# Kernel tuning notes

Hardware: AMD Instinct MI355X
Metric: run time of the kernel (lower is better)

The kernel has to match this reference:

```python
import jax, jax.numpy as jnp
import numpy as np
from jax import lax

LEAK = 0.2
EPS = 1e-5
T = 20  # sequence_length


def _lrelu(x):
    return jnp.where(x >= 0, x, LEAK * x)


def _deconv(x, w, stride=2, k=4, p=1):
    # PyTorch ConvTranspose2d(weight [in,out,kH,kW], stride=2, pad=1) equivalent:
    # flip kernel spatially, swap in/out channels, use lhs_dilation.
    wt = jnp.flip(w, (2, 3)).transpose(1, 0, 2, 3)  # OIHW
    pad = k - 1 - p
    return lax.conv_general_dilated(
        x, wt, window_strides=(1, 1), padding=[(pad, pad), (pad, pad)],
        lhs_dilation=(stride, stride),
        dimension_numbers=('NCHW', 'OIHW', 'NCHW'))


def _bn(x, g, b):
    # BatchNorm2d, training mode (batch statistics, biased variance)
    m = x.mean((0, 2, 3), keepdims=True)
    v = x.var((0, 2, 3), keepdims=True)
    return (x - m) * lax.rsqrt(v + EPS) * g[None, :, None, None] + b[None, :, None, None]


def setup_inputs() -> dict:
    B, CD, MD, H, FF = 64, 128, 128, 256, 512
    ks = jax.random.split(jax.random.key(0), 32)
    rn = lambda k, sh, s=0.02: (s * jax.random.normal(k, sh)).astype(jnp.float32)
    return {
        'z_content': jax.random.normal(ks[0], (B, CD), jnp.float32),
        'z_motion': jax.random.normal(ks[1], (B, MD), jnp.float32),
        'W_h': rn(ks[2], (H, CD + MD)), 'b_h': jnp.zeros((H,), jnp.float32),
        'W_c': rn(ks[3], (H, CD + MD)), 'b_c': jnp.zeros((H,), jnp.float32),
        'W_ih': rn(ks[4], (4 * H, H)), 'W_hh': rn(ks[5], (4 * H, H)),
        'b_ih': jnp.zeros((4 * H,), jnp.float32), 'b_hh': jnp.zeros((4 * H,), jnp.float32),
        'W_f': rn(ks[6], (FF, H)), 'b_f': jnp.zeros((FF,), jnp.float32),
        'init_in': rn(ks[7], (1, H), 0.1),
        'fc_W': rn(ks[8], (256 * 4 * 4, FF + CD)), 'fc_b': jnp.zeros((256 * 16,), jnp.float32),
        'w0': rn(ks[9], (256, 128, 4, 4)), 'g0': jnp.ones((128,), jnp.float32), 'be0': jnp.zeros((128,), jnp.float32),
        'w1': rn(ks[10], (128, 64, 4, 4)), 'g1': jnp.ones((64,), jnp.float32), 'be1': jnp.zeros((64,), jnp.float32),
        'w2': rn(ks[11], (64, 32, 4, 4)), 'g2': jnp.ones((32,), jnp.float32), 'be2': jnp.zeros((32,), jnp.float32),
        'wf': rn(ks[12], (32, 1, 4, 4)), 'bf': jnp.zeros((1,), jnp.float32),
    }


def reference(z_content, z_motion, W_h, b_h, W_c, b_c, W_ih, W_hh, b_ih, b_hh,
              W_f, b_f, init_in, fc_W, fc_b, w0, g0, be0, w1, g1, be1,
              w2, g2, be2, wf, bf):
    B = z_content.shape[0]
    z = jnp.concatenate([z_content, z_motion], axis=-1)
    h0 = z @ W_h.T + b_h  # [B,H]
    c0 = z @ W_c.T + b_c
    x0 = jnp.broadcast_to(init_in, (B, init_in.shape[1]))
    bias = b_ih + b_hh

    def step(carry, _):
        x, h, c = carry
        gates = x @ W_ih.T + h @ W_hh.T + bias  # [B,4H], torch gate order i,f,g,o
        i, f, g, o = jnp.split(gates, 4, axis=-1)
        c_new = jax.nn.sigmoid(f) * c + jax.nn.sigmoid(i) * jnp.tanh(g)
        h_new = jax.nn.sigmoid(o) * jnp.tanh(c_new)
        return (h_new, h_new, c_new), h_new

    _, outs = lax.scan(step, (x0, h0, c0), None, length=T)  # [T,B,H]
    outs = outs.transpose(1, 0, 2)  # [B,T,H]

    ff = _lrelu(outs @ W_f.T + b_f)  # [B,T,FF]
    zc = jnp.broadcast_to(z_content[:, None, :], (B, T, z_content.shape[1]))
    feat = jnp.concatenate([ff, zc], axis=-1).reshape(B * T, -1)  # [B*T, FF+CD]

    h = _lrelu(feat @ fc_W.T + fc_b).reshape(B * T, 256, 4, 4)
    h = _lrelu(_bn(_deconv(h, w0), g0, be0))   # [B*T,128,8,8]
    h = _lrelu(_bn(_deconv(h, w1), g1, be1))   # [B*T,64,16,16]
    h = _lrelu(_bn(_deconv(h, w2), g2, be2))   # [B*T,32,32,32]
    out = jax.nn.sigmoid(_deconv(h, wf) + bf[None, :, None, None])  # [B*T,1,64,64]
    return out.reshape(B, T, *out.shape[1:])
```

## Files before the change

### kernel.cpp

```cpp
#include <hip/hip_runtime.h>
#include <hip/hip_bf16.h>
#include <math.h>

typedef __hip_bfloat16 bf16;
typedef __attribute__((ext_vector_type(8))) short bf16x8;
typedef __attribute__((ext_vector_type(4))) float f32x4;
typedef __attribute__((ext_vector_type(2))) float f32x2;

#define LRELU(v) ((v) > 0.f ? (v) : 0.2f*(v))

__device__ __forceinline__ float sig_f(float x){ return 1.f/(1.f + __expf(-x)); }
__device__ __forceinline__ float tanh_f(float x){
  float ax = fabsf(x);
  float e = __expf(-2.f*ax);
  float t = (1.f - e)/(1.f + e);
  return x >= 0.f ? t : -t;
}
__device__ __forceinline__ ushort bfbits(float v){
  bf16 b = __float2bfloat16(v);
  return *(ushort*)&b;
}
__device__ __forceinline__ uint bfpack(float a, float b){
  return (uint)bfbits(a) | ((uint)bfbits(b) << 16);
}
__device__ __forceinline__ float bflo(uint u){ return __uint_as_float(u << 16); }
__device__ __forceinline__ float bfhi(uint u){ return __uint_as_float(u & 0xffff0000u); }

template<int CI, int CO>
__device__ __forceinline__ void wprep_body(const float* __restrict__ w,
                                           ushort* __restrict__ wpn, int e){
  constexpr int K = 4*CI, KF = K/32, MMW2 = CO/16;
  if (e >= 16*CI*CO) return;
  int j  = e & 7;
  int lk = (e >> 3) & 3;
  int lm = (e >> 5) & 15;
  int r3 = e >> 9;
  int kf = r3 % KF; int r4 = r3 / KF;
  int m  = r4 % MMW2; int p = r4 / MMW2;
  int k  = kf*32 + lk*8 + j;
  int t  = k / CI, ci = k % CI;
  int co = m*16 + lm;
  int py = p >> 1, px = p & 1, dy = t >> 1, dx = t & 1;
  int ky = (py ? 0 : 1) + 2*dy;
  int kx = (px ? 0 : 1) + 2*dx;
  wpn[e] = bfbits(w[((ci*CO + co)*4 + ky)*4 + kx]);
}

__global__ __launch_bounds__(256) void k_prep(
    const float* __restrict__ W_h, const float* __restrict__ W_c,
    float* __restrict__ WhT, float* __restrict__ WcT,
    const float* __restrict__ fc_W, ushort* __restrict__ wpfc,
    const float* __restrict__ W_f, ushort* __restrict__ wpff,
    const float* __restrict__ Wih, const float* __restrict__ Whh,
    uint4* __restrict__ Whq8, uint4* __restrict__ Wsq8, float* __restrict__ stats,
    const float* __restrict__ b_ih, const float* __restrict__ b_hh,
    const float* __restrict__ init_in,
    float4* __restrict__ xg4, float4* __restrict__ bias4,
    const float* __restrict__ w0, ushort* __restrict__ wp0,
    const float* __restrict__ w1, ushort* __restrict__ wp1,
    const float* __restrict__ w2, ushort* __restrict__ wp2,
    const float* __restrict__ wf, ushort* __restrict__ wfb)
{
  __shared__ float t[32][33];
  __shared__ float4 red[4];
  const int b = blockIdx.x, tid = threadIdx.x;

  if (b < 128) {
    const float* src = (b < 64) ? W_h : W_c;
    float* dst = (b < 64) ? WhT : WcT;
    int bb = b & 63;
    int c0 = (bb & 7)*32, r0 = (bb >> 3)*32;
    int tx = tid & 31, ty = tid >> 5;
    #pragma unroll
    for (int i = 0; i < 4; ++i)
      t[ty+8*i][tx] = src[(size_t)(r0+ty+8*i)*256 + c0+tx];
    __syncthreads();
    #pragma unroll
    for (int i = 0; i < 4; ++i)
      dst[(size_t)(c0+ty+8*i)*256 + r0+tx] = t[tx][ty+8*i];
    return;
  }
  if (b < 10368) {
    int i = (b - 128)*256 + tid;
    if (i < 2621440) wpfc[i] = bfbits(fc_W[i]);
    return;
  }
  if (b < 10880) {
    int i = (b - 10368)*256 + tid;
    if (i < 131072) wpff[i] = bfbits(W_f[i]);
    return;
  }
  if (b < 10944) {
    int k4 = b - 10880, j = tid;
    if (k4 < 2) { int i = k4*256 + j; if (i < 448) stats[i] = 0.f; }
    uint h4[4], s4[4];
    #pragma unroll
    for (int d = 0; d < 4; ++d) {
      int k = 4*k4 + d;
      float hi = Whh[j*256+k],       hf = Whh[(256+j)*256+k];
      float hg = Whh[(512+j)*256+k], ho = Whh[(768+j)*256+k];
      float ii = Wih[j*256+k],       iff = Wih[(256+j)*256+k];
      float ig = Wih[(512+j)*256+k], io = Wih[(768+j)*256+k];
      int lo = __builtin_amdgcn_cvt_pk_fp8_f32(hi, hf, 0, false);
      h4[d] = (uint)__builtin_amdgcn_cvt_pk_fp8_f32(hg, ho, lo, true);
      lo = __builtin_amdgcn_cvt_pk_fp8_f32(hi+ii, hf+iff, 0, false);
      s4[d] = (uint)__builtin_amdgcn_cvt_pk_fp8_f32(hg+ig, ho+io, lo, true);
    }
    Whq8[k4*256+j] = make_uint4(h4[0], h4[1], h4[2], h4[3]);
    Wsq8[k4*256+j] = make_uint4(s4[0], s4[1], s4[2], s4[3]);
    return;
  }
  if (b < 11200) {
    int bb = b - 10944, tt = tid;
    float v = init_in[tt];
    float p0 = v * Wih[bb*256 + tt];
    float p1 = v * Wih[(256+bb)*256 + tt];
    float p2 = v * Wih[(512+bb)*256 + tt];
    float p3 = v * Wih[(768+bb)*256 + tt];
    #pragma unroll
    for (int o = 32; o; o >>= 1) {
      p0 += __shfl_xor(p0, o); p1 += __shfl_xor(p1, o);
      p2 += __shfl_xor(p2, o); p3 += __shfl_xor(p3, o);
    }
    int lane = tt & 63, wid = tt >> 6;
    if (lane == 0) red[wid] = make_float4(p0,p1,p2,p3);
    __syncthreads();
    if (tt == 0) {
      float4 bi = make_float4(b_ih[bb]+b_hh[bb], b_ih[256+bb]+b_hh[256+bb],
                              b_ih[512+bb]+b_hh[512+bb], b_ih[768+bb]+b_hh[768+bb]);
      bias4[bb] = bi;
      float4 a = bi;
      #pragma unroll
      for (int w = 0; w < 4; ++w) { a.x += red[w].x; a.y += red[w].y; a.z += red[w].z; a.w += red[w].w; }
      xg4[bb] = a;
    }
    return;
  }
  if (b < 13248) { wprep_body<256,128>(w0, wp0, (b - 11200)*256 + tid); return; }
  if (b < 13760) { wprep_body<128,64>(w1, wp1, (b - 13248)*256 + tid); return; }
  if (b < 13888) { wprep_body<64,32>(w2, wp2, (b - 13760)*256 + tid); return; }
  {
    int e = (b - 13888)*256 + tid;
    if (e < 512) {
      int tt = e >> 5, ci = e & 31;
      wfb[tt*32 + ci] = bfbits(wf[ci*16 + tt]);
    }
  }
}

__global__ __launch_bounds__(256) void k_h0c0(const float* __restrict__ zc, const float* __restrict__ zm,
                      const float* __restrict__ WhT, const float* __restrict__ WcT,
                      const float* __restrict__ b_h, const float* __restrict__ b_c,
                      float* __restrict__ h, float* __restrict__ c){
  __shared__ float zs[256];
  int b = blockIdx.x, j = threadIdx.x;
  zs[j] = (j < 128) ? zc[b*128 + j] : zm[b*128 + (j-128)];
  __syncthreads();
  float ah = b_h[j], ac = b_c[j];
  #pragma unroll 4
  for (int k = 0; k < 256; ++k) {
    float zv = zs[k];
    ah = fmaf(zv, WhT[k*256 + j], ah);
    ac = fmaf(zv, WcT[k*256 + j], ac);
  }
  h[b*256+j] = ah; c[b*256+j] = ac;
}

__global__ __launch_bounds__(1024) void k_lstm_all(
    const uint4* __restrict__ Whq8, const uint4* __restrict__ Wsq8,
    const float4* __restrict__ xg4, const float4* __restrict__ bias4,
    const float* __restrict__ h0, const float* __restrict__ c0,
    ushort* __restrict__ outsb){
  __shared__ float hs[256];
  __shared__ float4 part[3][256];
  const int b = blockIdx.x, tid = threadIdx.x;
  const int j = tid & 255, kq = tid >> 8;
  float cj = 0.f;
  if (kq == 0) { hs[j] = h0[b*256 + j]; cj = c0[b*256 + j]; }
  __syncthreads();
  for (int t = 0; t < 20; ++t) {
    const uint4* __restrict__ Wp = ((t == 0) ? Whq8 : Wsq8) + (size_t)(kq*16)*256 + j;
    float4 a = make_float4(0.f, 0.f, 0.f, 0.f);
    #pragma unroll 8
    for (int kk = 0; kk < 16; ++kk) {
      uint4 wv = Wp[(size_t)kk*256];
      const float* __restrict__ hb = &hs[kq*64 + 4*kk];
      {
        f32x2 pif = __builtin_amdgcn_cvt_pk_f32_fp8((int)wv.x, false);
        f32x2 pgo = __builtin_amdgcn_cvt_pk_f32_fp8((int)wv.x, true);
        float hv = hb[0];
        a.x = fmaf(hv, pif[0], a.x); a.y = fmaf(hv, pif[1], a.y);
        a.z = fmaf(hv, pgo[0], a.z); a.w = fmaf(hv, pgo[1], a.w);
      }
      {
        f32x2 pif = __builtin_amdgcn_cvt_pk_f32_fp8((int)wv.y, false);
        f32x2 pgo = __builtin_amdgcn_cvt_pk_f32_fp8((int)wv.y, true);
        float hv = hb[1];
        a.x = fmaf(hv, pif[0], a.x); a.y = fmaf(hv, pif[1], a.y);
        a.z = fmaf(hv, pgo[0], a.z); a.w = fmaf(hv, pgo[1], a.w);
      }
      {
        f32x2 pif = __builtin_amdgcn_cvt_pk_f32_fp8((int)wv.z, false);
        f32x2 pgo = __builtin_amdgcn_cvt_pk_f32_fp8((int)wv.z, true);
        float hv = hb[2];
        a.x = fmaf(hv, pif[0], a.x); a.y = fmaf(hv, pif[1], a.y);
        a.z = fmaf(hv, pgo[0], a.z); a.w = fmaf(hv, pgo[1], a.w);
      }
      {
        f32x2 pif = __builtin_amdgcn_cvt_pk_f32_fp8((int)wv.w, false);
        f32x2 pgo = __builtin_amdgcn_cvt_pk_f32_fp8((int)wv.w, true);
        float hv = hb[3];
        a.x = fmaf(hv, pif[0], a.x); a.y = fmaf(hv, pif[1], a.y);
        a.z = fmaf(hv, pgo[0], a.z); a.w = fmaf(hv, pgo[1], a.w);
      }
    }
    if (kq) part[kq-1][j] = a;
    __syncthreads();
    if (kq == 0) {
      float4 p1 = part[0][j], p2 = part[1][j], p3 = part[2][j];
      float4 bb = (t == 0) ? xg4[j] : bias4[j];
      a.x += p1.x + p2.x + p3.x + bb.x;
      a.y += p1.y + p2.y + p3.y + bb.y;
      a.z += p1.z + p2.z + p3.z + bb.z;
      a.w += p1.w + p2.w + p3.w + bb.w;
      float ig = sig_f(a.x), fg = sig_f(a.y), gg = tanh_f(a.z), og = sig_f(a.w);
      cj = fmaf(fg, cj, ig*gg);
      float hj = og * tanh_f(cj);
      outsb[(b*20 + t)*256 + j] = bfbits(hj);
      hs[j] = hj;
    }
    __syncthreads();
  }
}

__global__ __launch_bounds__(256) void k_ff_m(
    const ushort* __restrict__ A, const ushort* __restrict__ W,
    const float* __restrict__ bias, const float* __restrict__ zc,
    ushort* __restrict__ C)
{
  constexpr int K = 256, BK = 64, NK = K/BK, BM = 128, BN = 64;
  constexpr int RS = 72;
  constexpr int NCF = BN/16;
  constexpr int AC = 4, WC = 2;

  __shared__ __align__(16) ushort Al[2][BM*RS];
  __shared__ __align__(16) ushort Wl[2][BN*RS];

  const int tid = threadIdx.x;
  const int col0 = blockIdx.x * BN, row0 = blockIdx.y * BM;
  const int w = tid >> 6, l = tid & 63, lm = l & 15, lk = l >> 4;

  f32x4 acc[NCF][2];
  #pragma unroll
  for (int m = 0; m < NCF; ++m)
    #pragma unroll
    for (int s = 0; s < 2; ++s)
      acc[m][s] = (f32x4){0.f,0.f,0.f,0.f};

  uint4 ar[AC], wr[WC];

  #define LOADG(kt) { \
    _Pragma("unroll") \
    for (int i = 0; i < AC; ++i) { \
      int chunk = tid + i*256; \
      int rl = chunk >> 3, kc = chunk & 7; \
      ar[i] = *(const uint4*)&A[(size_t)(row0+rl)*K + (kt)*BK + kc*8]; \
    } \
    _Pragma("unroll") \
    for (int i = 0; i < WC; ++i) { \
      int chunk = tid + i*256; \
      int co = chunk >> 3, kc = chunk & 7; \
      wr[i] = *(const uint4*)&W[(size_t)(col0+co)*K + (kt)*BK + kc*8]; \
    } }

  #define STOREL(buf) { \
    _Pragma("unroll") \
    for (int i = 0; i < AC; ++i) { \
      int chunk = tid + i*256; \
      int rl = chunk >> 3, kc = chunk & 7; \
      *(uint4*)&Al[buf][rl*RS + kc*8] = ar[i]; \
    } \
    _Pragma("unroll") \
    for (int i = 0; i < WC; ++i) { \
      int chunk = tid + i*256; \
      int co = chunk >> 3, kc = chunk & 7; \
      *(uint4*)&Wl[buf][co*RS + kc*8] = wr[i]; \
    } }

  LOADG(0);
  STOREL(0);
  int cur = 0;
  for (int kt = 0; kt < NK; ++kt) {
    if (kt + 1 < NK) LOADG(kt + 1);
    __syncthreads();
    #pragma unroll
    for (int kf = 0; kf < 2; ++kf) {
      bf16x8 bfr[2];
      #pragma unroll
      for (int s = 0; s < 2; ++s)
        bfr[s] = *(bf16x8*)&Al[cur][(w*32 + s*16 + lm)*RS + kf*32 + lk*8];
      #pragma unroll
      for (int m = 0; m < NCF; ++m) {
        bf16x8 afr = *(bf16x8*)&Wl[cur][(m*16 + lm)*RS + kf*32 + lk*8];
        acc[m][0] = __builtin_amdgcn_mfma_f32_16x16x32_bf16(afr, bfr[0], acc[m][0], 0, 0, 0);
        acc[m][1] = __builtin_amdgcn_mfma_f32_16x16x32_bf16(afr, bfr[1], acc[m][1], 0, 0, 0);
      }
    }
    if (kt + 1 < NK) STOREL(cur ^ 1);
    cur ^= 1;
  }

  #pragma unroll
  for (int m = 0; m < NCF; ++m) {
    #pragma unroll
    for (int s = 0; s < 2; ++s) {
      int row = row0 + w*32 + s*16 + lm;
      f32x4 v = acc[m][s];
      int u0 = col0 + m*16 + lk*4;
      union { ushort u[4]; uint2 q; } pk;
      #pragma unroll
      for (int j = 0; j < 4; ++j)
        pk.u[j] = bfbits(LRELU(v[j] + bias[u0+j]));
      *(uint2*)&C[(size_t)row*640 + u0] = pk.q;
    }
  }
  {
    int base = ((int)blockIdx.y*8 + (int)blockIdx.x)*2048 + tid;
    #pragma unroll
    for (int i = 0; i < 8; ++i) {
      int e = base + i*256;
      int r = e >> 7, c2 = e & 127;
      C[r*640 + 512 + c2] = bfbits(zc[(r/20)*128 + c2]);
    }
  }
  #undef LOADG
  #undef STOREL
}

__global__ __launch_bounds__(256) void k_gemm_fc_m(
    const ushort* __restrict__ A, const ushort* __restrict__ W,
    const float* __restrict__ bias, ushort* __restrict__ C)
{
  constexpr int K = 640, BK = 64, NK = K/BK, BM = 128, BN = 64;
  constexpr int RS = 72;
  constexpr int NCF = BN/16;
  constexpr int AC = 4, WC = 2;

  __shared__ __align__(16) ushort Al[2][BM*RS];
  __shared__ __align__(16) ushort Wl[2][BN*RS];

  const int tid = threadIdx.x;
  const int col0 = blockIdx.x * BN, row0 = blockIdx.y * BM;
  const int w = tid >> 6, l = tid & 63, lm = l & 15, lk = l >> 4;

  f32x4 acc[NCF][2];
  #pragma unroll
  for (int m = 0; m < NCF; ++m)
    #pragma unroll
    for (int s = 0; s < 2; ++s)
      acc[m][s] = (f32x4){0.f,0.f,0.f,0.f};

  uint4 ar[AC], wr[WC];

  #define LOADG(kt) { \
    _Pragma("unroll") \
    for (int i = 0; i < AC; ++i) { \
      int chunk = tid + i*256; \
      int rl = chunk >> 3, kc = chunk & 7; \
      ar[i] = *(const uint4*)&A[(size_t)(row0+rl)*K + (kt)*BK + kc*8]; \
    } \
    _Pragma("unroll") \
    for (int i = 0; i < WC; ++i) { \
      int chunk = tid + i*256; \
      int co = chunk >> 3, kc = chunk & 7; \
      wr[i] = *(const uint4*)&W[(size_t)(col0+co)*K + (kt)*BK + kc*8]; \
    } }

  #define STOREL(buf) { \
    _Pragma("unroll") \
    for (int i = 0; i < AC; ++i) { \
      int chunk = tid + i*256; \
      int rl = chunk >> 3, kc = chunk & 7; \
      *(uint4*)&Al[buf][rl*RS + kc*8] = ar[i]; \
    } \
    _Pragma("unroll") \
    for (int i = 0; i < WC; ++i) { \
      int chunk = tid + i*256; \
      int co = chunk >> 3, kc = chunk & 7; \
      *(uint4*)&Wl[buf][co*RS + kc*8] = wr[i]; \
    } }

  LOADG(0);
  STOREL(0);
  int cur = 0;
  for (int kt = 0; kt < NK; ++kt) {
    if (kt + 1 < NK) LOADG(kt + 1);
    __syncthreads();
    #pragma unroll
    for (int kf = 0; kf < 2; ++kf) {
      bf16x8 bfr[2];
      #pragma unroll
      for (int s = 0; s < 2; ++s)
        bfr[s] = *(bf16x8*)&Al[cur][(w*32 + s*16 + lm)*RS + kf*32 + lk*8];
      #pragma unroll
      for (int m = 0; m < NCF; ++m) {
        bf16x8 afr = *(bf16x8*)&Wl[cur][(m*16 + lm)*RS + kf*32 + lk*8];
        acc[m][0] = __builtin_amdgcn_mfma_f32_16x16x32_bf16(afr, bfr[0], acc[m][0], 0, 0, 0);
        acc[m][1] = __builtin_amdgcn_mfma_f32_16x16x32_bf16(afr, bfr[1], acc[m][1], 0, 0, 0);
      }
    }
    if (kt + 1 < NK) STOREL(cur ^ 1);
    cur ^= 1;
  }

  #pragma unroll
  for (int m = 0; m < NCF; ++m) {
    #pragma unroll
    for (int s = 0; s < 2; ++s) {
      int row = row0 + w*32 + s*16 + lm;
      f32x4 v = acc[m][s];
      #pragma unroll
      for (int j = 0; j < 4; ++j) {
        int u = col0 + m*16 + lk*4 + j;
        float val = LRELU(v[j] + bias[u]);
        C[((size_t)row << 12) + ((size_t)(u & 15) << 8) + (u >> 4)] = bfbits(val);
      }
    }
  }
  #undef LOADG
  #undef STOREL
}

template<int CI, int CO, int HI>
__global__ __attribute__((amdgpu_flat_work_group_size(256, 256), amdgpu_waves_per_eu(2, 4)))
void k_dcv(
    const ushort* __restrict__ in, const ushort* __restrict__ wp,
    ushort* __restrict__ out, float* __restrict__ gsum, float* __restrict__ gsq)
{
  constexpr int WI = HI, HO = 2*HI, WO = 2*WI;
  constexpr int K = 4*CI, BK = 64, NK = K/BK, KFT = K/32;
  constexpr int BSP = 128;
  constexpr int RS = 72;
  constexpr int NCF = CO/32;
  constexpr int COH = CO/2;
  constexpr int AC = BSP/32;

  __shared__ __align__(16) ushort Al[2][BSP*RS];
  __shared__ float s_sum[COH], s_sq[COH];

  const int tid = threadIdx.x;
  const int sp0 = blockIdx.x * BSP;
  const int p  = blockIdx.y;
  const int coz = blockIdx.z;
  const int py = p >> 1, px = p & 1;
  const int w  = tid >> 6, l = tid & 63;
  const int lm = l & 15, lk = l >> 4;

  if (tid < COH) { s_sum[tid] = 0.f; s_sq[tid] = 0.f; }

  f32x4 acc[NCF][2];
  #pragma unroll
  for (int m = 0; m < NCF; ++m)
    #pragma unroll
    for (int s = 0; s < 2; ++s)
      acc[m][s] = (f32x4){0.f,0.f,0.f,0.f};

  uint4 ar[AC];
  const ushort* wpb = wp + (size_t)(p*(CO/16) + coz*NCF)*KFT*512;

  #define LOADT(kt) { \
    int t = ((kt)*BK)/CI, ci0 = ((kt)*BK)%CI; \
    int dy = t >> 1, dx = t & 1; \
    _Pragma("unroll") \
    for (int i = 0; i < AC; ++i) { \
      int chunk = tid + i*256; \
      int rl = chunk >> 3, kc = chunk & 7; \
      int r = sp0 + rl; \
      int n = r / (HI*WI), rem = r % (HI*WI); \
      int oy = rem / WI, ox = rem % WI; \
      int iy = oy + py - dy, ix = ox + px - dx; \
      if ((unsigned)iy < (unsigned)HI && (unsigned)ix < (unsigned)WI) \
        ar[i] = *(const uint4*)&in[((((size_t)n*HI + iy)*WI + ix)*CI) + ci0 + kc*8]; \
      else ar[i] = make_uint4(0,0,0,0); \
    } }

  #define STORET(buf) { \
    _Pragma("unroll") \
    for (int i = 0; i < AC; ++i) { \
      int chunk = tid + i*256; \
      int rl = chunk >> 3, kc = chunk & 7; \
      *(uint4*)&Al[buf][rl*RS + kc*8] = ar[i]; \
    } }

  LOADT(0);
  STORET(0);
  bf16x8 afrN[NCF];
  #pragma unroll
  for (int m = 0; m < NCF; ++m)
    afrN[m] = *(const bf16x8*)&wpb[((size_t)m*KFT)*512 + lm*32 + lk*8];
  int cur = 0;
  for (int kt = 0; kt < NK; ++kt) {
    if (kt + 1 < NK) LOADT(kt + 1);
    __syncthreads();
    #pragma unroll
    for (int kf = 0; kf < 2; ++kf) {
      const int ktg = kt*2 + kf;
      bf16x8 afr[NCF];
      #pragma unroll
      for (int m = 0; m < NCF; ++m) afr[m] = afrN[m];
      if (ktg + 1 < KFT) {
        #pragma unroll
        for (int m = 0; m < NCF; ++m)
          afrN[m] = *(const bf16x8*)&wpb[((size_t)m*KFT + ktg + 1)*512 + lm*32 + lk*8];
      }
      bf16x8 bfr[2];
      #pragma unroll
      for (int s = 0; s < 2; ++s)
        bfr[s] = *(bf16x8*)&Al[cur][(w*32 + s*16 + lm)*RS + kf*32 + lk*8];
      #pragma unroll
      for (int m = 0; m < NCF; ++m) {
        acc[m][0] = __builtin_amdgcn_mfma_f32_16x16x32_bf16(afr[m], bfr[0], acc[m][0], 0, 0, 0);
        acc[m][1] = __builtin_amdgcn_mfma_f32_16x16x32_bf16(afr[m], bfr[1], acc[m][1], 0, 0, 0);
      }
    }
    if (kt + 1 < NK) STORET(cur ^ 1);
    cur ^= 1;
  }

  #pragma unroll
  for (int m = 0; m < NCF; ++m) {
    float s1[4] = {0,0,0,0}, s2[4] = {0,0,0,0};
    #pragma unroll
    for (int s = 0; s < 2; ++s) {
      f32x4 v = acc[m][s];
      #pragma unroll
      for (int j = 0; j < 4; ++j) { s1[j] += v[j]; s2[j] += v[j]*v[j]; }
    }
    #pragma unroll
    for (int j = 0; j < 4; ++j) {
      float a = s1[j], b = s2[j];
      #pragma unroll
      for (int o = 1; o < 16; o <<= 1) { a += __shfl_xor(a, o); b += __shfl_xor(b, o); }
      if (lm == 0) {
        atomicAdd(&s_sum[m*16 + lk*4 + j], a);
        atomicAdd(&s_sq [m*16 + lk*4 + j], b);
      }
    }
  }
  #pragma unroll
  for (int s = 0; s < 2; ++s) {
    int sp = sp0 + w*32 + s*16 + lm;
    int n = sp / (HI*WI), rem = sp % (HI*WI);
    int y = 2*(rem / WI) + py, x = 2*(rem % WI) + px;
    size_t ob = (((size_t)n*HO + y)*WO + x)*CO + coz*COH + lk*4;
    #pragma unroll
    for (int m = 0; m < NCF; ++m) {
      f32x4 v = acc[m][s];
      union { ushort u[4]; uint2 q; } pk;
      pk.u[0] = bfbits(v[0]); pk.u[1] = bfbits(v[1]);
      pk.u[2] = bfbits(v[2]); pk.u[3] = bfbits(v[3]);
      *(uint2*)&out[ob + m*16] = pk.q;
    }
  }
  __syncthreads();
  for (int cc = tid; cc < COH; cc += 256) {
    atomicAdd(&gsum[coz*COH + cc], s_sum[cc]);
    atomicAdd(&gsq[coz*COH + cc],  s_sq[cc]);
  }
  #undef LOADT
  #undef STORET
}

template<int CI, int CO, int HI>
__global__ __attribute__((amdgpu_flat_work_group_size(512, 512), amdgpu_waves_per_eu(2, 4)))
void k_dcvim(
    const ushort* __restrict__ in, const ushort* __restrict__ wp,
    const float* __restrict__ gsumP, const float* __restrict__ gsqP,
    const float* __restrict__ gP, const float* __restrict__ beP, float invNP,
    ushort* __restrict__ out, float* __restrict__ gsum, float* __restrict__ gsq)
{
  constexpr int WI = HI, HO = 2*HI, WO = 2*WI;
  constexpr int K = 4*CI;
  constexpr int KF = K/32;
  constexpr int PAD = HI + 2;
  constexpr int CICH = CI/8;
  constexpr int MMW2 = CO/16;
  constexpr int SFTH = HI*WI/32;

  __shared__ __align__(16) ushort Ain[PAD*PAD*CI];
  __shared__ float s_sum[CO], s_sq[CO];
  __shared__ float s_scale[CI], s_shift[CI];

  const int tid = threadIdx.x;
  const int n = blockIdx.x;
  const int w = tid >> 6, l = tid & 63, lm = l & 15, lk = l >> 4;
  const int p = w >> 1, py = p >> 1, px = p & 1, ph = w & 1;

  if (tid < CO) { s_sum[tid] = 0.f; s_sq[tid] = 0.f; }
  if (tid >= 512-CI) {
    int c = tid - (512-CI);
    float m = gsumP[c]*invNP;
    float v = gsqP[c]*invNP - m*m;
    float sc = gP[c]*rsqrtf(v + 1e-5f);
    s_scale[c] = sc;
    s_shift[c] = beP[c] - m*sc;
  }
  __syncthreads();

  const ushort* inb = in + (size_t)n * HI * WI * CI;
  constexpr int NPCH = PAD*PAD*CICH;
  for (int e = tid; e < NPCH; e += 512) {
    int ci8 = e % CICH; int sp = e / CICH;
    int c = sp % PAD, r = sp / PAD;
    int chS = ci8 ^ (c & 7);
    if (r >= 1 && r <= HI && c >= 1 && c <= WI) {
      uint4 u = *(const uint4*)&inb[(((size_t)(r-1)*WI + (c-1))*CI) + ci8*8];
      int ci0 = ci8*8;
      float4 sc0 = *(const float4*)&s_scale[ci0];
      float4 sc1 = *(const float4*)&s_scale[ci0+4];
      float4 sh0 = *(const float4*)&s_shift[ci0];
      float4 sh1 = *(const float4*)&s_shift[ci0+4];
      float v0 = LRELU(fmaf(bflo(u.x), sc0.x, sh0.x));
      float v1 = LRELU(fmaf(bfhi(u.x), sc0.y, sh0.y));
      float v2 = LRELU(fmaf(bflo(u.y), sc0.z, sh0.z));
      float v3 = LRELU(fmaf(bfhi(u.y), sc0.w, sh0.w));
      float v4 = LRELU(fmaf(bflo(u.z), sc1.x, sh1.x));
      float v5 = LRELU(fmaf(bfhi(u.z), sc1.y, sh1.y));
      float v6 = LRELU(fmaf(bflo(u.w), sc1.z, sh1.z));
      float v7 = LRELU(fmaf(bfhi(u.w), sc1.w, sh1.w));
      uint4 o;
      o.x = (uint)bfpack(v0, v1);
      o.y = (uint)bfpack(v2, v3);
      o.z = (uint)bfpack(v4, v5);
      o.w = (uint)bfpack(v6, v7);
      ((uint4*)Ain)[(r*PAD + c)*CICH + chS] = o;
    } else {
      ((uint4*)Ain)[(r*PAD + c)*CICH + chS] = make_uint4(0,0,0,0);
    }
  }
  __syncthreads();

  f32x4 acc[MMW2][SFTH];
  #pragma unroll
  for (int m = 0; m < MMW2; ++m)
    #pragma unroll
    for (int sf = 0; sf < SFTH; ++sf)
      acc[m][sf] = (f32x4){0.f,0.f,0.f,0.f};

  const ushort* wpb = wp + (size_t)(p*MMW2)*KF*512;
  bf16x8 afrN[MMW2];
  #pragma unroll
  for (int m = 0; m < MMW2; ++m)
    afrN[m] = *(const bf16x8*)&wpb[((size_t)m*KF)*512 + lm*32 + lk*8];
  #pragma unroll
  for (int kf = 0; kf < KF; ++kf) {
    const int t = (kf*32)/CI, cib = (kf*32)%CI;
    const int dy = t >> 1, dx = t & 1;
    bf16x8 afr[MMW2];
    #pragma unroll
    for (int m = 0; m < MMW2; ++m) afr[m] = afrN[m];
    if (kf + 1 < KF) {
      #pragma unroll
      for (int m = 0; m < MMW2; ++m)
        afrN[m] = *(const bf16x8*)&wpb[((size_t)m*KF + (kf+1))*512 + lm*32 + lk*8];
    }
    const int ch = (cib >> 3) + lk;
    #pragma unroll
    for (int sf = 0; sf < SFTH; ++sf) {
      int s = (ph*SFTH + sf)*16 + lm;
      int y = s / WI, x = s % WI;
      int r = y + py - dy + 1, c = x + px - dx + 1;
      bf16x8 bfr = *(const bf16x8*)&Ain[((r*PAD + c)*CICH + (ch ^ (c & 7)))*8];
      #pragma unroll
      for (int m = 0; m < MMW2; ++m)
        acc[m][sf] = __builtin_amdgcn_mfma_f32_16x16x32_bf16(afr[m], bfr, acc[m][sf], 0, 0, 0);
    }
  }

  float s1[MMW2][4], s2[MMW2][4];
  #pragma unroll
  for (int m = 0; m < MMW2; ++m)
    #pragma unroll
    for (int j = 0; j < 4; ++j) { s1[m][j] = 0.f; s2[m][j] = 0.f; }

  #pragma unroll
  for (int sf = 0; sf < SFTH; ++sf) {
    int s = (ph*SFTH + sf)*16 + lm;
    int y = 2*(s / WI) + py, x = 2*(s % WI) + px;
    size_t ob = (((size_t)n*HO + y)*WO + x)*CO + lk*4;
    #pragma unroll
    for (int m = 0; m < MMW2; ++m) {
      f32x4 v = acc[m][sf];
      union { ushort u[4]; uint2 q; } pk;
      #pragma unroll
      for (int j = 0; j < 4; ++j) {
        pk.u[j] = bfbits(v[j]);
        s1[m][j] += v[j];
        s2[m][j] += v[j]*v[j];
      }
      *(uint2*)&out[ob + m*16] = pk.q;
    }
  }

  #pragma unroll
  for (int m = 0; m < MMW2; ++m) {
    #pragma unroll
    for (int j = 0; j < 4; ++j) {
      float a = s1[m][j], b = s2[m][j];
      #pragma unroll
      for (int o = 1; o < 16; o <<= 1) { a += __shfl_xor(a, o); b += __shfl_xor(b, o); }
      if (lm == 0) {
        atomicAdd(&s_sum[m*16 + lk*4 + j], a);
        atomicAdd(&s_sq [m*16 + lk*4 + j], b);
      }
    }
  }

  __syncthreads();
  for (int cc = tid; cc < CO; cc += 512) {
    atomicAdd(&gsum[cc], s_sum[cc]);
    atomicAdd(&gsq[cc],  s_sq[cc]);
  }
}

__global__ __launch_bounds__(256) void k_final(
    const ushort* __restrict__ in, const ushort* __restrict__ wfb,
    const float* __restrict__ gsumP, const float* __restrict__ gsqP,
    const float* __restrict__ gP, const float* __restrict__ beP, float invNP,
    const float* __restrict__ bfb, float* __restrict__ outp)
{
  constexpr int CI=32, HI=32, WI=32, HO=64, WO=64, SPLIT=4, HOq=HO/SPLIT;
  constexpr int RMAX = 10;
  constexpr int DP = 20;
  __shared__ float Dl[RMAX*32*DP];
  __shared__ float s_scale[CI], s_shift[CI];

  const int tid = threadIdx.x, bid = blockIdx.x;
  const int n = bid % 1280, q = bid / 1280;
  const int y0 = q * HOq;
  const int rows_lo = max(0, y0/2 - 1);
  const int rows_hi = min(HI-1, (y0 + HOq)/2);
  const int nrows = rows_hi - rows_lo + 1;

  if (tid < CI) {
    float m = gsumP[tid]*invNP;
    float v = gsqP[tid]*invNP - m*m;
    float sc = gP[tid]*rsqrtf(v + 1e-5f);
    s_scale[tid] = sc;
    s_shift[tid] = beP[tid] - m*sc;
  }
  __syncthreads();

  const int w = tid >> 6, l = tid & 63, lm = l & 15, lk = l >> 4;
  const bf16x8 afr = *(const bf16x8*)&wfb[lm*32 + lk*8];
  const float4 sc0 = *(const float4*)&s_scale[lk*8];
  const float4 sc1 = *(const float4*)&s_scale[lk*8+4];
  const float4 sh0 = *(const float4*)&s_shift[lk*8];
  const float4 sh1 = *(const float4*)&s_shift[lk*8+4];

  const ushort* inb = in + (size_t)n * HI * WI * CI;
  const int ngrp = nrows * 2;
  for (int g = w; g < ngrp; g += 4) {
    int px = g*16 + lm;
    int rl = px >> 5, ix = px & 31;
    uint4 u = *(const uint4*)&inb[(((size_t)(rows_lo+rl)*WI + ix)*CI) + lk*8];
    float v0 = LRELU(fmaf(bflo(u.x), sc0.x, sh0.x));
    float v1 = LRELU(fmaf(bfhi(u.x), sc0.y, sh0.y));
    float v2 = LRELU(fmaf(bflo(u.y), sc0.z, sh0.z));
    float v3 = LRELU(fmaf(bfhi(u.y), sc0.w, sh0.w));
    float v4 = LRELU(fmaf(bflo(u.z), sc1.x, sh1.x));
    float v5 = LRELU(fmaf(bfhi(u.z), sc1.y, sh1.y));
    float v6 = LRELU(fmaf(bflo(u.w), sc1.z, sh1.z));
    float v7 = LRELU(fmaf(bfhi(u.w), sc1.w, sh1.w));
    union { uint uu[4]; bf16x8 v; } pk;
    pk.uu[0] = bfpack(v0, v1);
    pk.uu[1] = bfpack(v2, v3);
    pk.uu[2] = bfpack(v4, v5);
    pk.uu[3] = bfpack(v6, v7);
    f32x4 d = __builtin_amdgcn_mfma_f32_16x16x32_bf16(afr, pk.v, (f32x4){0.f,0.f,0.f,0.f}, 0, 0, 0);
    *(f32x4*)&Dl[px*DP + lk*4] = d;
  }
  __syncthreads();

  const float b0 = bfb[0];
  #pragma unroll
  for (int i = 0; i < (HOq*WO)/256; ++i) {
    int e = tid + i*256;
    int oy = e >> 6, x = e & 63;
    int y = y0 + oy;
    int kya = (y + 1) & 1, iya = (y + 1) >> 1;
    int kxa = (x + 1) & 1, ixa = (x + 1) >> 1;
    float acc = b0;
    #pragma unroll
    for (int dy = 0; dy < 2; ++dy) {
      int iy = iya - dy, ky = kya + 2*dy;
      if (iy < 0 || iy >= HI) continue;
      #pragma unroll
      for (int dx = 0; dx < 2; ++dx) {
        int ix = ixa - dx, kx = kxa + 2*dx;
        if (ix < 0 || ix >= WI) continue;
        acc += Dl[((iy - rows_lo)*WI + ix)*DP + (ky*4 + kx)];
      }
    }
    outp[(size_t)n*HO*WO + y*WO + x] = 1.f/(1.f + __expf(-acc));
  }
}

extern "C" void kernel_launch(void* const* d_in, const int* in_sizes, int n_in,
                              void* d_out, int out_size, void* d_ws, size_t ws_size,
                              hipStream_t stream) {
  const float* z_content = (const float*)d_in[0];
  const float* z_motion  = (const float*)d_in[1];
  const float* W_h  = (const float*)d_in[2];
  const float* b_h  = (const float*)d_in[3];
  const float* W_c  = (const float*)d_in[4];
  const float* b_c  = (const float*)d_in[5];
  const float* W_ih = (const float*)d_in[6];
  const float* W_hh = (const float*)d_in[7];
  const float* b_ih = (const float*)d_in[8];
  const float* b_hh = (const float*)d_in[9];
  const float* W_f  = (const float*)d_in[10];
  const float* b_f  = (const float*)d_in[11];
  const float* init_in = (const float*)d_in[12];
  const float* fc_W = (const float*)d_in[13];
  const float* fc_b = (const float*)d_in[14];
  const float* w0 = (const float*)d_in[15];
  const float* g0 = (const float*)d_in[16];
  const float* be0 = (const float*)d_in[17];
  const float* w1 = (const float*)d_in[18];
  const float* g1 = (const float*)d_in[19];
  const float* be1 = (const float*)d_in[20];
  const float* w2 = (const float*)d_in[21];
  const float* g2 = (const float*)d_in[22];
  const float* be2 = (const float*)d_in[23];
  const float* wf = (const float*)d_in[24];
  const float* bf_ = (const float*)d_in[25];

  const size_t P_BYTES = 10631168;
  const size_t X_OFF   = P_BYTES;
  const size_t X_BYTES = 83886080;
  const size_t Y_OFF   = X_OFF + X_BYTES;
  const size_t NEED    = Y_OFF + 41943040;
  if (ws_size < NEED) return;

  float* ws = (float*)d_ws;
  char*  wsb = (char*)d_ws;
  float* sum0 = ws + 0;        float* sq0 = ws + 128;
  float* sum1 = ws + 256;      float* sq1 = ws + 320;
  float* sum2 = ws + 384;      float* sq2 = ws + 416;
  float4* xg4   = (float4*)(ws + 1024);
  float4* bias4 = (float4*)(ws + 2048);
  float* h    = ws + 3072;
  float* c    = ws + 19456;
  ushort* outsb = (ushort*)(ws + 35840);
  float* WhT  = ws + 199680;
  float* WcT  = ws + 265216;
  uint4* Whq8 = (uint4*)(ws + 330752);
  uint4* Wsq8 = (uint4*)(ws + 592896);
  ushort* wp0 = (ushort*)(ws + 855040);
  ushort* wp1 = (ushort*)(ws + 1117184);
  ushort* wp2 = (ushort*)(ws + 1182720);
  ushort* wfb = (ushort*)(ws + 1199104);
  ushort* wpff = (ushort*)(ws + 1199616);
  ushort* featb = (ushort*)(ws + 1265152);

  ushort* wpfc = (ushort*)(wsb + X_OFF);
  ushort* out0 = (ushort*)(wsb + X_OFF);
  ushort* out2 = (ushort*)(wsb + X_OFF);
  ushort* h1   = (ushort*)(wsb + Y_OFF);
  ushort* out1 = (ushort*)(wsb + Y_OFF);

  k_prep<<<13890, 256, 0, stream>>>(
      W_h, W_c, WhT, WcT, fc_W, wpfc, W_f, wpff,
      W_ih, W_hh, Whq8, Wsq8, ws, b_ih, b_hh, init_in, xg4, bias4,
      w0, wp0, w1, wp1, w2, wp2, wf, wfb);
  k_h0c0<<<64, 256, 0, stream>>>(z_content, z_motion, WhT, WcT, b_h, b_c, h, c);

  k_lstm_all<<<64, 1024, 0, stream>>>(Whq8, Wsq8, xg4, bias4, h, c, outsb);

  k_ff_m<<<dim3(8, 10), 256, 0, stream>>>(outsb, wpff, b_f, z_content, featb);
  k_gemm_fc_m<<<dim3(64, 10), 256, 0, stream>>>(featb, wpfc, fc_b, h1);

  k_dcv<256,128,4><<<dim3(160,4,2), 256, 0, stream>>>(h1, wp0, out0, sum0, sq0);
  k_dcvim<128,64,8><<<1280, 512, 0, stream>>>(out0, wp1, sum0, sq0, g0, be0, 1.f/81920.f, out1, sum1, sq1);
  k_dcvim<64,32,16><<<1280, 512, 0, stream>>>(out1, wp2, sum1, sq1, g1, be1, 1.f/327680.f, out2, sum2, sq2);
  k_final<<<5120, 256, 0, stream>>>(out2, wfb, sum2, sq2, g2, be2, 1.f/1310720.f, bf_, (float*)d_out);
}
```

Measured before the change: 400.8 us.

## Load deconv B fragments directly from global, drop LDS staging in k_dcv

The k_dcv deconvolution GEMM kernel no longer stages the im2col activation tile through double-buffered shared memory with barriers. Each lane now reads its own bf16x8 input fragment straight from global memory per k-step, using spatial coordinates computed once up front. This removes LDS traffic, the per-iteration __syncthreads, and the shared-memory footprint, which may raise occupancy. In exchange, the global loads are no longer prefetched a tile ahead, so load latency can stall the MFMAs unless other waves hide it.

```diff
diff --git a/kernel.cpp b/kernel.cpp
--- a/kernel.cpp
+++ b/kernel.cpp
@@ -438,14 +438,11 @@
     ushort* __restrict__ out, float* __restrict__ gsum, float* __restrict__ gsq)
 {
   constexpr int WI = HI, HO = 2*HI, WO = 2*WI;
-  constexpr int K = 4*CI, BK = 64, NK = K/BK, KFT = K/32;
+  constexpr int K = 4*CI, KFT = K/32;
   constexpr int BSP = 128;
-  constexpr int RS = 72;
   constexpr int NCF = CO/32;
   constexpr int COH = CO/2;
-  constexpr int AC = BSP/32;
-
-  __shared__ __align__(16) ushort Al[2][BSP*RS];
+
   __shared__ float s_sum[COH], s_sq[COH];
 
   const int tid = threadIdx.x;
@@ -465,66 +462,49 @@
     for (int s = 0; s < 2; ++s)
       acc[m][s] = (f32x4){0.f,0.f,0.f,0.f};
 
-  uint4 ar[AC];
+  int pn[2], poy[2], pox[2];
+  #pragma unroll
+  for (int s = 0; s < 2; ++s) {
+    int sp = sp0 + w*32 + s*16 + lm;
+    pn[s] = sp / (HI*WI);
+    int rem = sp % (HI*WI);
+    poy[s] = rem / WI; pox[s] = rem % WI;
+  }
+
   const ushort* wpb = wp + (size_t)(p*(CO/16) + coz*NCF)*KFT*512;
 
-  #define LOADT(kt) { \
-    int t = ((kt)*BK)/CI, ci0 = ((kt)*BK)%CI; \
-    int dy = t >> 1, dx = t & 1; \
-    _Pragma("unroll") \
-    for (int i = 0; i < AC; ++i) { \
-      int chunk = tid + i*256; \
-      int rl = chunk >> 3, kc = chunk & 7; \
-      int r = sp0 + rl; \
-      int n = r / (HI*WI), rem = r % (HI*WI); \
-      int oy = rem / WI, ox = rem % WI; \
-      int iy = oy + py - dy, ix = ox + px - dx; \
-      if ((unsigned)iy < (unsigned)HI && (unsigned)ix < (unsigned)WI) \
-        ar[i] = *(const uint4*)&in[((((size_t)n*HI + iy)*WI + ix)*CI) + ci0 + kc*8]; \
-      else ar[i] = make_uint4(0,0,0,0); \
-    } }
-
-  #define STORET(buf) { \
-    _Pragma("unroll") \
-    for (int i = 0; i < AC; ++i) { \
-      int chunk = tid + i*256; \
-      int rl = chunk >> 3, kc = chunk & 7; \
-      *(uint4*)&Al[buf][rl*RS + kc*8] = ar[i]; \
-    } }
-
-  LOADT(0);
-  STORET(0);
   bf16x8 afrN[NCF];
   #pragma unroll
   for (int m = 0; m < NCF; ++m)
     afrN[m] = *(const bf16x8*)&wpb[((size_t)m*KFT)*512 + lm*32 + lk*8];
-  int cur = 0;
-  for (int kt = 0; kt < NK; ++kt) {
-    if (kt + 1 < NK) LOADT(kt + 1);
-    __syncthreads();
-    #pragma unroll
-    for (int kf = 0; kf < 2; ++kf) {
-      const int ktg = kt*2 + kf;
-      bf16x8 afr[NCF];
-      #pragma unroll
-      for (int m = 0; m < NCF; ++m) afr[m] = afrN[m];
-      if (ktg + 1 < KFT) {
-        #pragma unroll
-        for (int m = 0; m < NCF; ++m)
-          afrN[m] = *(const bf16x8*)&wpb[((size_t)m*KFT + ktg + 1)*512 + lm*32 + lk*8];
-      }
-      bf16x8 bfr[2];
-      #pragma unroll
-      for (int s = 0; s < 2; ++s)
-        bfr[s] = *(bf16x8*)&Al[cur][(w*32 + s*16 + lm)*RS + kf*32 + lk*8];
-      #pragma unroll
-      for (int m = 0; m < NCF; ++m) {
-        acc[m][0] = __builtin_amdgcn_mfma_f32_16x16x32_bf16(afr[m], bfr[0], acc[m][0], 0, 0, 0);
-        acc[m][1] = __builtin_amdgcn_mfma_f32_16x16x32_bf16(afr[m], bfr[1], acc[m][1], 0, 0, 0);
-      }
-    }
-    if (kt + 1 < NK) STORET(cur ^ 1);
-    cur ^= 1;
+
+  for (int ktg = 0; ktg < KFT; ++ktg) {
+    const int t = (ktg*32)/CI;
+    const int ci0 = (ktg*32)%CI + lk*8;
+    const int dy = t >> 1, dx = t & 1;
+    bf16x8 afr[NCF];
+    #pragma unroll
+    for (int m = 0; m < NCF; ++m) afr[m] = afrN[m];
+    if (ktg + 1 < KFT) {
+      #pragma unroll
+      for (int m = 0; m < NCF; ++m)
+        afrN[m] = *(const bf16x8*)&wpb[((size_t)m*KFT + ktg + 1)*512 + lm*32 + lk*8];
+    }
+    bf16x8 bfr[2];
+    #pragma unroll
+    for (int s = 0; s < 2; ++s) {
+      int iy = poy[s] + py - dy, ix = pox[s] + px - dx;
+      bool valid = ((unsigned)iy < (unsigned)HI) && ((unsigned)ix < (unsigned)WI);
+      if (valid)
+        bfr[s] = *(const bf16x8*)&in[((((size_t)pn[s]*HI + iy)*WI + ix)*CI) + ci0];
+      else
+        bfr[s] = (bf16x8){0,0,0,0,0,0,0,0};
+    }
+    #pragma unroll
+    for (int m = 0; m < NCF; ++m) {
+      acc[m][0] = __builtin_amdgcn_mfma_f32_16x16x32_bf16(afr[m], bfr[0], acc[m][0], 0, 0, 0);
+      acc[m][1] = __builtin_amdgcn_mfma_f32_16x16x32_bf16(afr[m], bfr[1], acc[m][1], 0, 0, 0);
+    }
   }
 
   #pragma unroll
@@ -549,10 +529,8 @@
   }
   #pragma unroll
   for (int s = 0; s < 2; ++s) {
-    int sp = sp0 + w*32 + s*16 + lm;
-    int n = sp / (HI*WI), rem = sp % (HI*WI);
-    int y = 2*(rem / WI) + py, x = 2*(rem % WI) + px;
-    size_t ob = (((size_t)n*HO + y)*WO + x)*CO + coz*COH + lk*4;
+    int y = 2*poy[s] + py, x = 2*pox[s] + px;
+    size_t ob = (((size_t)pn[s]*HO + y)*WO + x)*CO + coz*COH + lk*4;
     #pragma unroll
     for (int m = 0; m < NCF; ++m) {
       f32x4 v = acc[m][s];
@@ -567,8 +545,6 @@
     atomicAdd(&gsum[coz*COH + cc], s_sum[cc]);
     atomicAdd(&gsq[coz*COH + cc],  s_sq[cc]);
   }
-  #undef LOADT
-  #undef STORET
 }
 
 template<int CI, int CO, int HI>
```

Measured after the change: 414.2 us. 1.03x slower.
